# Optimization experiments

Measured on AMD Instinct MI355X. Metric: run time of the kernel, lower is better.

Reference implementation:

```python
import jax, jax.numpy as jnp
import numpy as np

B, T, D, H = 128, 64, 1024, 16
HD = D // H  # head dim = 64, matches smolgen per-pair bias last dim


def setup_inputs() -> dict:
    key = jax.random.key(0)
    ks = jax.random.split(key, 8)
    w = 0.02  # RandomNormal(stddev=0.02) init used throughout the repo
    return {
        "x": jax.random.normal(ks[0], (B, T, D), jnp.float32),
        # per-pair smolgen biases, shared across heads: [B, T, T, head_dim]
        "a_q": jax.random.normal(ks[1], (B, T, T, HD), jnp.float32) * 0.1,
        "a_k": jax.random.normal(ks[2], (B, T, T, HD), jnp.float32) * 0.1,
        "a_v": jax.random.normal(ks[3], (B, T, T, HD), jnp.float32) * 0.1,
        "Wq": jax.random.normal(ks[4], (D, D), jnp.float32) * w,
        "Wk": jax.random.normal(ks[5], (D, D), jnp.float32) * w,
        "Wv": jax.random.normal(ks[6], (D, D), jnp.float32) * w,
        "Wo": jax.random.normal(ks[7], (D, D), jnp.float32) * w,
    }


def reference(x, a_q, a_k, a_v, Wq, Wk, Wv, Wo):
    b, t, d_model = x.shape
    q = (x @ Wq).reshape(b, t, H, HD)
    k = (x @ Wk).reshape(b, t, H, HD)
    v = (x @ Wv).reshape(b, t, H, HD)
    scale = 1.0 / np.sqrt(HD).astype(np.float32)
    # standard content-content logits
    logits = jnp.einsum("bqhd,bkhd->bhqk", q, k) * scale
    # additive per-pair smolgen biases folded into QK^T (broadcast over heads)
    logits = logits + jnp.einsum("bqkd,bkhd->bhqk", a_q, k)
    logits = logits + jnp.einsum("bqhd,bqkd->bhqk", q, a_k)
    probs = jax.nn.softmax(logits, axis=-1)
    out = jnp.einsum("bhqk,bkhd->bqhd", probs, v)
    # per-pair value bias gathered by attention weights
    out = out + jnp.einsum("bhqk,bqkd->bqhd", probs, a_v)
    return out.reshape(b, t, d_model) @ Wo
```

## Files before the change

### kernel.cpp

```cpp
#include <hip/hip_runtime.h>
#include <hip/hip_bf16.h>

#define Bn 128
#define Tn 64
#define Dn 1024
#define Hn 16
#define HDn 64

typedef __bf16 bf16_t;
typedef __bf16 bf16x8 __attribute__((ext_vector_type(8)));
typedef float f32x4 __attribute__((ext_vector_type(4)));

__device__ __forceinline__ f32x4 mfma16(bf16x8 a, bf16x8 b, f32x4 c) {
  return __builtin_amdgcn_mfma_f32_16x16x32_bf16(a, b, c, 0, 0, 0);
}

__device__ __forceinline__ bf16x8 ld8f(const float* p) {
  float4 a = *(const float4*)p;
  float4 b = *(const float4*)(p + 4);
  bf16x8 r;
  r[0] = (bf16_t)a.x; r[1] = (bf16_t)a.y; r[2] = (bf16_t)a.z; r[3] = (bf16_t)a.w;
  r[4] = (bf16_t)b.x; r[5] = (bf16_t)b.y; r[6] = (bf16_t)b.z; r[7] = (bf16_t)b.w;
  return r;
}

__global__ __launch_bounds__(256) void convert_bf16(const float* __restrict__ src,
                                                    bf16_t* __restrict__ dst) {
  long i = ((long)blockIdx.x * 256 + threadIdx.x) * 8;
  *(bf16x8*)(dst + i) = ld8f(src + i);
}

__global__ __launch_bounds__(256) void transpose_mat(const float* __restrict__ W,
                                                     bf16_t* __restrict__ Wt) {
  __shared__ bf16_t tile[64][65];
  const int tr = blockIdx.y, tc = blockIdx.x;
  const int t = threadIdx.x;
#pragma unroll
  for (int i = 0; i < 16; i++) {
    int idx = t + i * 256;
    int r = idx >> 6, c = idx & 63;
    tile[r][c] = (bf16_t)W[(long)(tr * 64 + r) * 1024 + tc * 64 + c];
  }
  __syncthreads();
#pragma unroll
  for (int i = 0; i < 16; i++) {
    int idx = t + i * 256;
    int c = idx >> 6, r = idx & 63;
    Wt[(long)(tc * 64 + c) * 1024 + tr * 64 + r] = tile[r][c];
  }
}

template <typename CT>
__global__ __launch_bounds__(256) void gemm_bt(const bf16_t* __restrict__ A,
                                               const bf16_t* __restrict__ Bt,
                                               CT* __restrict__ C,
                                               int M, int N, int K) {
  __shared__ bf16_t As[128 * 64];
  __shared__ bf16_t Bs[128 * 64];
  const int t = threadIdx.x;
  const int w = t >> 6, lane = t & 63;
  const int l16 = lane & 15, quad = lane >> 4;
  const int m0 = blockIdx.y * 128, n0 = blockIdx.x * 128;
  const int wm = (w >> 1) * 64, wn = (w & 1) * 64;

  f32x4 acc[4][4];
#pragma unroll
  for (int i = 0; i < 4; i++)
#pragma unroll
    for (int j = 0; j < 4; j++) acc[i][j] = (f32x4){0.f, 0.f, 0.f, 0.f};

  const int sr = t >> 3;
  const int sc = (t & 7) * 8;

  for (int k0 = 0; k0 < K; k0 += 64) {
    __syncthreads();
#pragma unroll
    for (int i = 0; i < 4; i++) {
      int row = i * 32 + sr;
      *(bf16x8*)(As + row * 64 + sc) =
          *(const bf16x8*)(A + (long)(m0 + row) * K + k0 + sc);
      *(bf16x8*)(Bs + row * 64 + sc) =
          *(const bf16x8*)(Bt + (long)(n0 + row) * K + k0 + sc);
    }
    __syncthreads();
#pragma unroll
    for (int kk = 0; kk < 64; kk += 32) {
      bf16x8 af[4], bfr[4];
#pragma unroll
      for (int i = 0; i < 4; i++)
        af[i] = *(const bf16x8*)(As + (wm + i * 16 + l16) * 64 + kk + quad * 8);
#pragma unroll
      for (int j = 0; j < 4; j++)
        bfr[j] = *(const bf16x8*)(Bs + (wn + j * 16 + l16) * 64 + kk + quad * 8);
#pragma unroll
      for (int i = 0; i < 4; i++)
#pragma unroll
        for (int j = 0; j < 4; j++) acc[i][j] = mfma16(af[i], bfr[j], acc[i][j]);
    }
  }
#pragma unroll
  for (int i = 0; i < 4; i++)
#pragma unroll
    for (int j = 0; j < 4; j++) {
      int col = n0 + wn + j * 16 + l16;
#pragma unroll
      for (int r = 0; r < 4; r++) {
        int row = m0 + wm + i * 16 + quad * 4 + r;
        C[(long)row * N + col] = (CT)acc[i][j][r];
      }
    }
}

__global__ __launch_bounds__(256) void logits_cc(const bf16_t* __restrict__ Q,
                                                 const bf16_t* __restrict__ Km,
                                                 float* __restrict__ logits) {
  const int h = blockIdx.x, b = blockIdx.y;
  const int t = threadIdx.x, w = t >> 6, lane = t & 63;
  const int l16 = lane & 15, quad = lane >> 4;
  const bf16_t* qbase = Q + (long)b * (Tn * Dn) + h * HDn;
  const bf16_t* kbase = Km + (long)b * (Tn * Dn) + h * HDn;
  f32x4 acc[4];
#pragma unroll
  for (int j = 0; j < 4; j++) acc[j] = (f32x4){0.f, 0.f, 0.f, 0.f};
#pragma unroll
  for (int kk = 0; kk < 64; kk += 32) {
    bf16x8 af = *(const bf16x8*)(qbase + (long)(w * 16 + l16) * Dn + kk + quad * 8);
#pragma unroll
    for (int j = 0; j < 4; j++) {
      bf16x8 bfr = *(const bf16x8*)(kbase + (long)(j * 16 + l16) * Dn + kk + quad * 8);
      acc[j] = mfma16(af, bfr, acc[j]);
    }
  }
  float* lb = logits + ((long)(b * Hn + h) * Tn) * Tn;
#pragma unroll
  for (int j = 0; j < 4; j++)
#pragma unroll
    for (int r = 0; r < 4; r++) {
      int q = w * 16 + quad * 4 + r, k = j * 16 + l16;
      lb[q * 64 + k] = acc[j][r] * 0.125f;
    }
}

__global__ __launch_bounds__(256) void logits_aq(const float* __restrict__ aqp,
                                                 const bf16_t* __restrict__ Km,
                                                 float* __restrict__ logits) {
  const int b = blockIdx.y;
  const int kfix = blockIdx.x * 4 + (threadIdx.x >> 6);
  const int lane = threadIdx.x & 63, l16 = lane & 15, quad = lane >> 4;
  const float* abase = aqp + (long)b * (Tn * Tn * HDn) + kfix * HDn;
  const bf16_t* bbase = Km + (long)(b * Tn + kfix) * Dn;
  f32x4 acc[4];
#pragma unroll
  for (int i = 0; i < 4; i++) acc[i] = (f32x4){0.f, 0.f, 0.f, 0.f};
#pragma unroll
  for (int kk = 0; kk < 64; kk += 32) {
    bf16x8 bfr = *(const bf16x8*)(bbase + l16 * 64 + kk + quad * 8);
#pragma unroll
    for (int i = 0; i < 4; i++) {
      bf16x8 af = ld8f(abase + (long)(i * 16 + l16) * (Tn * HDn) + kk + quad * 8);
      acc[i] = mfma16(af, bfr, acc[i]);
    }
  }
  float* lb = logits + (long)b * (Hn * Tn * Tn) + kfix;
#pragma unroll
  for (int i = 0; i < 4; i++)
#pragma unroll
    for (int r = 0; r < 4; r++) {
      int q = i * 16 + quad * 4 + r, h = l16;
      lb[(long)h * (Tn * Tn) + q * Tn] += acc[i][r];
    }
}

__global__ __launch_bounds__(256) void logits_ak(const bf16_t* __restrict__ Q,
                                                 const float* __restrict__ akp,
                                                 float* __restrict__ logits) {
  const int b = blockIdx.y;
  const int q = blockIdx.x * 4 + (threadIdx.x >> 6);
  const int lane = threadIdx.x & 63, l16 = lane & 15, quad = lane >> 4;
  const bf16_t* abase = Q + (long)(b * Tn + q) * Dn;
  const float* bbase = akp + (long)(b * Tn + q) * (Tn * HDn);
  f32x4 acc[4];
#pragma unroll
  for (int j = 0; j < 4; j++) acc[j] = (f32x4){0.f, 0.f, 0.f, 0.f};
#pragma unroll
  for (int kk = 0; kk < 64; kk += 32) {
    bf16x8 af = *(const bf16x8*)(abase + l16 * 64 + kk + quad * 8);
#pragma unroll
    for (int j = 0; j < 4; j++) {
      bf16x8 bfr = ld8f(bbase + (long)(j * 16 + l16) * 64 + kk + quad * 8);
      acc[j] = mfma16(af, bfr, acc[j]);
    }
  }
  float* lb = logits + (long)b * (Hn * Tn * Tn) + q * 64;
#pragma unroll
  for (int j = 0; j < 4; j++)
#pragma unroll
    for (int r = 0; r < 4; r++) {
      int h = quad * 4 + r, k = j * 16 + l16;
      lb[(long)h * (Tn * Tn) + k] += acc[j][r];
    }
}

__global__ __launch_bounds__(256) void softmax_pav(const float* __restrict__ logits,
                                                   const float* __restrict__ avp,
                                                   bf16_t* __restrict__ probs,
                                                   bf16_t* __restrict__ out2) {
  const int q = blockIdx.x, b = blockIdx.y;
  __shared__ bf16_t pl[16][72];
  __shared__ bf16_t avT[64][72];
  const int t = threadIdx.x, w = t >> 6, lane = t & 63;
  const int l16 = lane & 15, quad = lane >> 4;

  {
    const float* src = avp + (long)(b * Tn + q) * (Tn * HDn);
    int k = t >> 2, d0 = (t & 3) * 16;
    unsigned short* lds = (unsigned short*)&avT[0][0];
#pragma unroll
    for (int c = 0; c < 4; c++) {
      float4 v = *(const float4*)(src + k * 64 + d0 + c * 4);
      bf16_t e0 = (bf16_t)v.x, e1 = (bf16_t)v.y, e2 = (bf16_t)v.z, e3 = (bf16_t)v.w;
      lds[(d0 + c * 4 + 0) * 72 + k] = *(unsigned short*)&e0;
      lds[(d0 + c * 4 + 1) * 72 + k] = *(unsigned short*)&e1;
      lds[(d0 + c * 4 + 2) * 72 + k] = *(unsigned short*)&e2;
      lds[(d0 + c * 4 + 3) * 72 + k] = *(unsigned short*)&e3;
    }
  }

  const int k = lane;
#pragma unroll
  for (int i = 0; i < 4; i++) {
    int h = w * 4 + i;
    float val = logits[((long)(b * Hn + h) * Tn + q) * Tn + k];
    float m = val;
#pragma unroll
    for (int off = 32; off; off >>= 1) m = fmaxf(m, __shfl_xor(m, off));
    float e = __expf(val - m);
    float s = e;
#pragma unroll
    for (int off = 32; off; off >>= 1) s += __shfl_xor(s, off);
    float p = e / s;
    bf16_t pb = (bf16_t)p;
    probs[((long)(b * Hn + h) * Tn + q) * Tn + k] = pb;
    pl[h][k] = pb;
  }
  __syncthreads();

  f32x4 acc = (f32x4){0.f, 0.f, 0.f, 0.f};
#pragma unroll
  for (int kk = 0; kk < 64; kk += 32) {
    bf16x8 af = *(const bf16x8*)(&pl[l16][kk + quad * 8]);
    bf16x8 bfr = *(const bf16x8*)(&avT[w * 16 + l16][kk + quad * 8]);
    acc = mfma16(af, bfr, acc);
  }
  bf16_t* ob = out2 + (long)(b * Tn + q) * Dn;
#pragma unroll
  for (int r = 0; r < 4; r++) {
    int h = quad * 4 + r, d = w * 16 + l16;
    ob[h * 64 + d] = (bf16_t)acc[r];
  }
}

__global__ __launch_bounds__(256) void pv_out(const bf16_t* __restrict__ probs,
                                              const bf16_t* __restrict__ V,
                                              const bf16_t* __restrict__ out2,
                                              bf16_t* __restrict__ attn) {
  const int h = blockIdx.x, b = blockIdx.y;
  __shared__ bf16_t VT[64][72];
  const int t = threadIdx.x, w = t >> 6, lane = t & 63;
  const int l16 = lane & 15, quad = lane >> 4;

  {
    const bf16_t* src = V + (long)b * (Tn * Dn) + h * HDn;
    int k = t & 63, d0 = (t >> 6) * 16;
    union { uint4 u; unsigned short s[8]; } v0, v1;
    v0.u = *(const uint4*)(src + (long)k * Dn + d0);
    v1.u = *(const uint4*)(src + (long)k * Dn + d0 + 8);
    unsigned short* lds = (unsigned short*)&VT[0][0];
#pragma unroll
    for (int j = 0; j < 8; j++) lds[(d0 + j) * 72 + k] = v0.s[j];
#pragma unroll
    for (int j = 0; j < 8; j++) lds[(d0 + 8 + j) * 72 + k] = v1.s[j];
  }
  __syncthreads();

  const bf16_t* pbase = probs + ((long)(b * Hn + h) * Tn) * Tn;
  f32x4 acc[4];
#pragma unroll
  for (int j = 0; j < 4; j++) acc[j] = (f32x4){0.f, 0.f, 0.f, 0.f};
#pragma unroll
  for (int kk = 0; kk < 64; kk += 32) {
    bf16x8 af = *(const bf16x8*)(pbase + (long)(w * 16 + l16) * Tn + kk + quad * 8);
#pragma unroll
    for (int j = 0; j < 4; j++) {
      bf16x8 bfr = *(const bf16x8*)(&VT[j * 16 + l16][kk + quad * 8]);
      acc[j] = mfma16(af, bfr, acc[j]);
    }
  }
#pragma unroll
  for (int j = 0; j < 4; j++)
#pragma unroll
    for (int r = 0; r < 4; r++) {
      int qrow = w * 16 + quad * 4 + r, d = j * 16 + l16;
      long idx = (long)(b * Tn + qrow) * Dn + h * HDn + d;
      attn[idx] = (bf16_t)(acc[j][r] + (float)out2[idx]);
    }
}

extern "C" void kernel_launch(void* const* d_in, const int* in_sizes, int n_in,
                              void* d_out, int out_size, void* d_ws, size_t ws_size,
                              hipStream_t stream) {
  const float* x  = (const float*)d_in[0];
  const float* aq = (const float*)d_in[1];
  const float* ak = (const float*)d_in[2];
  const float* av = (const float*)d_in[3];
  const float* Wq = (const float*)d_in[4];
  const float* Wk = (const float*)d_in[5];
  const float* Wv = (const float*)d_in[6];
  const float* Wo = (const float*)d_in[7];
  float* out = (float*)d_out;

  char* ws = (char*)d_ws;
  const size_t MB = 1024 * 1024;
  bf16_t* WqT    = (bf16_t*)(ws + 0 * MB);
  bf16_t* WkT    = (bf16_t*)(ws + 2 * MB);
  bf16_t* WvT    = (bf16_t*)(ws + 4 * MB);
  bf16_t* WoT    = (bf16_t*)(ws + 6 * MB);
  bf16_t* xb     = (bf16_t*)(ws + 8 * MB);
  bf16_t* Qb     = (bf16_t*)(ws + 24 * MB);
  bf16_t* Kb     = (bf16_t*)(ws + 40 * MB);
  bf16_t* Vb     = (bf16_t*)(ws + 56 * MB);
  float*  logits = (float*)(ws + 72 * MB);
  bf16_t* probs  = (bf16_t*)(ws + 104 * MB);
  bf16_t* out2   = (bf16_t*)(ws + 120 * MB);
  bf16_t* attn   = (bf16_t*)(ws + 136 * MB);

  dim3 blk(256);
  convert_bf16<<<dim3(4096), blk, 0, stream>>>(x, xb);
  transpose_mat<<<dim3(16, 16), blk, 0, stream>>>(Wq, WqT);
  transpose_mat<<<dim3(16, 16), blk, 0, stream>>>(Wk, WkT);
  transpose_mat<<<dim3(16, 16), blk, 0, stream>>>(Wv, WvT);
  transpose_mat<<<dim3(16, 16), blk, 0, stream>>>(Wo, WoT);

  gemm_bt<bf16_t><<<dim3(8, 64), blk, 0, stream>>>(xb, WqT, Qb, Bn * Tn, Dn, Dn);
  gemm_bt<bf16_t><<<dim3(8, 64), blk, 0, stream>>>(xb, WkT, Kb, Bn * Tn, Dn, Dn);
  gemm_bt<bf16_t><<<dim3(8, 64), blk, 0, stream>>>(xb, WvT, Vb, Bn * Tn, Dn, Dn);

  logits_cc<<<dim3(Hn, Bn), blk, 0, stream>>>(Qb, Kb, logits);
  logits_aq<<<dim3(16, Bn), blk, 0, stream>>>(aq, Kb, logits);
  logits_ak<<<dim3(16, Bn), blk, 0, stream>>>(Qb, ak, logits);

  softmax_pav<<<dim3(Tn, Bn), blk, 0, stream>>>(logits, av, probs, out2);
  pv_out<<<dim3(Hn, Bn), blk, 0, stream>>>(probs, Vb, out2, attn);

  gemm_bt<float><<<dim3(8, 64), blk, 0, stream>>>(attn, WoT, out, Bn * Tn, Dn, Dn);
}
```

Measured before the change: 649.2 us.

## Fuse logit bias terms, softmax and value-bias gather into one attention kernel

Replaces the three logit kernels and the softmax/value-bias kernel with a single 1024-thread kernel per (batch, 16-query tile). The fp32 logits now stay in shared memory instead of round-tripping through a 32 MB global buffer with read-modify-write passes. The kernel also uses swizzled LDS layouts for the probabilities and the transposed value bias. In exchange it uses large shared memory (about 100 KB) and 1024-thread blocks, which limits occupancy, and it adds several block-wide barriers.

```diff
diff --git a/kernel.cpp b/kernel.cpp
--- a/kernel.cpp
+++ b/kernel.cpp
@@ -111,152 +111,159 @@
     }
 }
 
-__global__ __launch_bounds__(256) void logits_cc(const bf16_t* __restrict__ Q,
-                                                 const bf16_t* __restrict__ Km,
-                                                 float* __restrict__ logits) {
-  const int h = blockIdx.x, b = blockIdx.y;
-  const int t = threadIdx.x, w = t >> 6, lane = t & 63;
-  const int l16 = lane & 15, quad = lane >> 4;
-  const bf16_t* qbase = Q + (long)b * (Tn * Dn) + h * HDn;
-  const bf16_t* kbase = Km + (long)b * (Tn * Dn) + h * HDn;
-  f32x4 acc[4];
-#pragma unroll
-  for (int j = 0; j < 4; j++) acc[j] = (f32x4){0.f, 0.f, 0.f, 0.f};
-#pragma unroll
-  for (int kk = 0; kk < 64; kk += 32) {
-    bf16x8 af = *(const bf16x8*)(qbase + (long)(w * 16 + l16) * Dn + kk + quad * 8);
-#pragma unroll
-    for (int j = 0; j < 4; j++) {
-      bf16x8 bfr = *(const bf16x8*)(kbase + (long)(j * 16 + l16) * Dn + kk + quad * 8);
-      acc[j] = mfma16(af, bfr, acc[j]);
-    }
-  }
-  float* lb = logits + ((long)(b * Hn + h) * Tn) * Tn;
-#pragma unroll
-  for (int j = 0; j < 4; j++)
-#pragma unroll
-    for (int r = 0; r < 4; r++) {
-      int q = w * 16 + quad * 4 + r, k = j * 16 + l16;
-      lb[q * 64 + k] = acc[j][r] * 0.125f;
-    }
-}
-
-__global__ __launch_bounds__(256) void logits_aq(const float* __restrict__ aqp,
-                                                 const bf16_t* __restrict__ Km,
-                                                 float* __restrict__ logits) {
-  const int b = blockIdx.y;
-  const int kfix = blockIdx.x * 4 + (threadIdx.x >> 6);
-  const int lane = threadIdx.x & 63, l16 = lane & 15, quad = lane >> 4;
-  const float* abase = aqp + (long)b * (Tn * Tn * HDn) + kfix * HDn;
-  const bf16_t* bbase = Km + (long)(b * Tn + kfix) * Dn;
-  f32x4 acc[4];
-#pragma unroll
-  for (int i = 0; i < 4; i++) acc[i] = (f32x4){0.f, 0.f, 0.f, 0.f};
-#pragma unroll
-  for (int kk = 0; kk < 64; kk += 32) {
-    bf16x8 bfr = *(const bf16x8*)(bbase + l16 * 64 + kk + quad * 8);
-#pragma unroll
-    for (int i = 0; i < 4; i++) {
-      bf16x8 af = ld8f(abase + (long)(i * 16 + l16) * (Tn * HDn) + kk + quad * 8);
-      acc[i] = mfma16(af, bfr, acc[i]);
-    }
-  }
-  float* lb = logits + (long)b * (Hn * Tn * Tn) + kfix;
-#pragma unroll
-  for (int i = 0; i < 4; i++)
-#pragma unroll
-    for (int r = 0; r < 4; r++) {
-      int q = i * 16 + quad * 4 + r, h = l16;
-      lb[(long)h * (Tn * Tn) + q * Tn] += acc[i][r];
-    }
-}
-
-__global__ __launch_bounds__(256) void logits_ak(const bf16_t* __restrict__ Q,
-                                                 const float* __restrict__ akp,
-                                                 float* __restrict__ logits) {
-  const int b = blockIdx.y;
-  const int q = blockIdx.x * 4 + (threadIdx.x >> 6);
-  const int lane = threadIdx.x & 63, l16 = lane & 15, quad = lane >> 4;
-  const bf16_t* abase = Q + (long)(b * Tn + q) * Dn;
-  const float* bbase = akp + (long)(b * Tn + q) * (Tn * HDn);
-  f32x4 acc[4];
-#pragma unroll
-  for (int j = 0; j < 4; j++) acc[j] = (f32x4){0.f, 0.f, 0.f, 0.f};
-#pragma unroll
-  for (int kk = 0; kk < 64; kk += 32) {
-    bf16x8 af = *(const bf16x8*)(abase + l16 * 64 + kk + quad * 8);
-#pragma unroll
-    for (int j = 0; j < 4; j++) {
-      bf16x8 bfr = ld8f(bbase + (long)(j * 16 + l16) * 64 + kk + quad * 8);
-      acc[j] = mfma16(af, bfr, acc[j]);
-    }
-  }
-  float* lb = logits + (long)b * (Hn * Tn * Tn) + q * 64;
-#pragma unroll
-  for (int j = 0; j < 4; j++)
-#pragma unroll
-    for (int r = 0; r < 4; r++) {
-      int h = quad * 4 + r, k = j * 16 + l16;
-      lb[(long)h * (Tn * Tn) + k] += acc[j][r];
-    }
-}
-
-__global__ __launch_bounds__(256) void softmax_pav(const float* __restrict__ logits,
-                                                   const float* __restrict__ avp,
-                                                   bf16_t* __restrict__ probs,
-                                                   bf16_t* __restrict__ out2) {
-  const int q = blockIdx.x, b = blockIdx.y;
-  __shared__ bf16_t pl[16][72];
-  __shared__ bf16_t avT[64][72];
-  const int t = threadIdx.x, w = t >> 6, lane = t & 63;
-  const int l16 = lane & 15, quad = lane >> 4;
-
-  {
-    const float* src = avp + (long)(b * Tn + q) * (Tn * HDn);
-    int k = t >> 2, d0 = (t & 3) * 16;
-    unsigned short* lds = (unsigned short*)&avT[0][0];
-#pragma unroll
-    for (int c = 0; c < 4; c++) {
-      float4 v = *(const float4*)(src + k * 64 + d0 + c * 4);
-      bf16_t e0 = (bf16_t)v.x, e1 = (bf16_t)v.y, e2 = (bf16_t)v.z, e3 = (bf16_t)v.w;
-      lds[(d0 + c * 4 + 0) * 72 + k] = *(unsigned short*)&e0;
-      lds[(d0 + c * 4 + 1) * 72 + k] = *(unsigned short*)&e1;
-      lds[(d0 + c * 4 + 2) * 72 + k] = *(unsigned short*)&e2;
-      lds[(d0 + c * 4 + 3) * 72 + k] = *(unsigned short*)&e3;
-    }
-  }
-
-  const int k = lane;
-#pragma unroll
-  for (int i = 0; i < 4; i++) {
-    int h = w * 4 + i;
-    float val = logits[((long)(b * Hn + h) * Tn + q) * Tn + k];
-    float m = val;
-#pragma unroll
-    for (int off = 32; off; off >>= 1) m = fmaxf(m, __shfl_xor(m, off));
-    float e = __expf(val - m);
-    float s = e;
-#pragma unroll
-    for (int off = 32; off; off >>= 1) s += __shfl_xor(s, off);
-    float p = e / s;
-    bf16_t pb = (bf16_t)p;
-    probs[((long)(b * Hn + h) * Tn + q) * Tn + k] = pb;
-    pl[h][k] = pb;
-  }
-  __syncthreads();
-
-  f32x4 acc = (f32x4){0.f, 0.f, 0.f, 0.f};
-#pragma unroll
-  for (int kk = 0; kk < 64; kk += 32) {
-    bf16x8 af = *(const bf16x8*)(&pl[l16][kk + quad * 8]);
-    bf16x8 bfr = *(const bf16x8*)(&avT[w * 16 + l16][kk + quad * 8]);
-    acc = mfma16(af, bfr, acc);
-  }
-  bf16_t* ob = out2 + (long)(b * Tn + q) * Dn;
-#pragma unroll
-  for (int r = 0; r < 4; r++) {
-    int h = quad * 4 + r, d = w * 16 + l16;
-    ob[h * 64 + d] = (bf16_t)acc[r];
+__global__ __launch_bounds__(1024) void fused_att(
+    const bf16_t* __restrict__ Qb, const bf16_t* __restrict__ Kb,
+    const float* __restrict__ aqp, const float* __restrict__ akp,
+    const float* __restrict__ avp,
+    bf16_t* __restrict__ probs, bf16_t* __restrict__ out2) {
+  __shared__ float Ls[256 * 65];
+  __shared__ bf16_t Pb[256 * 64];
+
+  const int id = blockIdx.x;
+  const int b = (id & 7) * 16 + ((id >> 3) & 15);
+  const int q0 = (id >> 7) * 16;
+  const int t = threadIdx.x;
+  const int w = t >> 6, lane = t & 63, l16 = lane & 15, quad = lane >> 4;
+
+  {
+    const int h = w;
+    f32x4 acc[4];
+#pragma unroll
+    for (int j = 0; j < 4; j++) acc[j] = (f32x4){0.f, 0.f, 0.f, 0.f};
+    const bf16_t* qb = Qb + (long)(b * Tn + q0 + l16) * Dn + h * HDn;
+    const bf16_t* kb = Kb + (long)b * (Tn * Dn) + h * HDn;
+#pragma unroll
+    for (int kk = 0; kk < 64; kk += 32) {
+      bf16x8 af = *(const bf16x8*)(qb + kk + quad * 8);
+#pragma unroll
+      for (int j = 0; j < 4; j++) {
+        bf16x8 bf = *(const bf16x8*)(kb + (long)(j * 16 + l16) * Dn + kk + quad * 8);
+        acc[j] = mfma16(af, bf, acc[j]);
+      }
+    }
+#pragma unroll
+    for (int j = 0; j < 4; j++)
+#pragma unroll
+      for (int r = 0; r < 4; r++)
+        Ls[((quad * 4 + r) * 16 + h) * 65 + j * 16 + l16] = 0.125f * acc[j][r];
+  }
+  __syncthreads();
+
+  {
+    const float* ab = aqp + (long)(b * Tn + q0 + l16) * (Tn * HDn);
+    const bf16_t* kb = Kb + (long)b * (Tn * Dn) + l16 * HDn;
+#pragma unroll
+    for (int kc = 0; kc < 4; kc++) {
+      const int k = w * 4 + kc;
+      f32x4 acc = (f32x4){0.f, 0.f, 0.f, 0.f};
+#pragma unroll
+      for (int kk = 0; kk < 64; kk += 32) {
+        bf16x8 af = ld8f(ab + k * HDn + kk + quad * 8);
+        bf16x8 bf = *(const bf16x8*)(kb + (long)k * Dn + kk + quad * 8);
+        acc = mfma16(af, bf, acc);
+      }
+#pragma unroll
+      for (int r = 0; r < 4; r++)
+        Ls[((quad * 4 + r) * 16 + l16) * 65 + k] += acc[r];
+    }
+  }
+  __syncthreads();
+
+  {
+    const int q = w;
+    const bf16_t* qb = Qb + (long)(b * Tn + q0 + q) * Dn + l16 * HDn;
+    const float* ab = akp + (long)(b * Tn + q0 + q) * (Tn * HDn);
+    f32x4 acc[4];
+#pragma unroll
+    for (int j = 0; j < 4; j++) acc[j] = (f32x4){0.f, 0.f, 0.f, 0.f};
+#pragma unroll
+    for (int kk = 0; kk < 64; kk += 32) {
+      bf16x8 af = *(const bf16x8*)(qb + kk + quad * 8);
+#pragma unroll
+      for (int j = 0; j < 4; j++) {
+        bf16x8 bf = ld8f(ab + (long)(j * 16 + l16) * HDn + kk + quad * 8);
+        acc[j] = mfma16(af, bf, acc[j]);
+      }
+    }
+#pragma unroll
+    for (int j = 0; j < 4; j++)
+#pragma unroll
+      for (int r = 0; r < 4; r++)
+        Ls[(q * 16 + quad * 4 + r) * 65 + j * 16 + l16] += acc[j][r];
+  }
+  __syncthreads();
+
+  {
+    const int r = t >> 2, qq = t & 3;
+    const int q = r >> 4, h = r & 15;
+    const float* row = Ls + r * 65 + qq * 16;
+    float m = -1e30f;
+#pragma unroll
+    for (int i = 0; i < 16; i++) m = fmaxf(m, row[i]);
+    m = fmaxf(m, __shfl_xor(m, 1));
+    m = fmaxf(m, __shfl_xor(m, 2));
+    float e[16];
+    float s = 0.f;
+#pragma unroll
+    for (int i = 0; i < 16; i++) { e[i] = __expf(row[i] - m); s += e[i]; }
+    s += __shfl_xor(s, 1);
+    s += __shfl_xor(s, 2);
+    const float inv = 1.0f / s;
+    const int swz = (q ^ h) & 7;
+    bf16_t* pr = probs + ((long)(b * Hn + h) * Tn + q0 + q) * Tn + qq * 16;
+#pragma unroll
+    for (int c = 0; c < 2; c++) {
+      bf16x8 v;
+#pragma unroll
+      for (int ee = 0; ee < 8; ee++) v[ee] = (bf16_t)(e[c * 8 + ee] * inv);
+      *(bf16x8*)(pr + c * 8) = v;
+      const int cg = qq * 2 + c;
+      *(bf16x8*)(Pb + r * 64 + (cg ^ swz) * 8) = v;
+    }
+  }
+
+  {
+    const int q = w;
+    bf16_t* avT = (bf16_t*)(Ls + 16 * w * 65);
+    const float* src = avp + (long)(b * Tn + q0 + q) * (Tn * HDn) + lane * HDn;
+    f32x4 acc[4];
+#pragma unroll
+    for (int j = 0; j < 4; j++) acc[j] = (f32x4){0.f, 0.f, 0.f, 0.f};
+    const int aswz = (q ^ l16) & 7;
+#pragma unroll
+    for (int half = 0; half < 2; half++) {
+      asm volatile("s_waitcnt lgkmcnt(0)" ::: "memory");
+#pragma unroll
+      for (int c = 0; c < 8; c++) {
+        float4 v = *(const float4*)(src + half * 32 + c * 4);
+#pragma unroll
+        for (int ee = 0; ee < 4; ee++) {
+          int dl = c * 4 + ee;
+          avT[dl * 64 + (((lane >> 3) ^ dl) & 7) * 8 + (lane & 7)] =
+              (bf16_t)(&v.x)[ee];
+        }
+      }
+      asm volatile("s_waitcnt lgkmcnt(0)" ::: "memory");
+      __builtin_amdgcn_sched_barrier(0);
+#pragma unroll
+      for (int kk = 0; kk < 64; kk += 32) {
+        const int cg = (kk >> 3) + quad;
+        bf16x8 af = *(const bf16x8*)(Pb + (q * 16 + l16) * 64 + (cg ^ aswz) * 8);
+#pragma unroll
+        for (int jj = 0; jj < 2; jj++) {
+          int j = half * 2 + jj;
+          int dl = jj * 16 + l16;
+          bf16x8 bf = *(const bf16x8*)(avT + dl * 64 + ((cg ^ (dl & 7))) * 8);
+          acc[j] = mfma16(af, bf, acc[j]);
+        }
+      }
+    }
+    bf16_t* ob = out2 + (long)(b * Tn + q0 + q) * Dn;
+#pragma unroll
+    for (int j = 0; j < 4; j++)
+#pragma unroll
+      for (int r = 0; r < 4; r++)
+        ob[(quad * 4 + r) * HDn + j * 16 + l16] = (bf16_t)acc[j][r];
   }
 }
 
@@ -329,10 +336,9 @@
   bf16_t* Qb     = (bf16_t*)(ws + 24 * MB);
   bf16_t* Kb     = (bf16_t*)(ws + 40 * MB);
   bf16_t* Vb     = (bf16_t*)(ws + 56 * MB);
-  float*  logits = (float*)(ws + 72 * MB);
-  bf16_t* probs  = (bf16_t*)(ws + 104 * MB);
-  bf16_t* out2   = (bf16_t*)(ws + 120 * MB);
-  bf16_t* attn   = (bf16_t*)(ws + 136 * MB);
+  bf16_t* probs  = (bf16_t*)(ws + 72 * MB);
+  bf16_t* out2   = (bf16_t*)(ws + 88 * MB);
+  bf16_t* attn   = (bf16_t*)(ws + 104 * MB);
 
   dim3 blk(256);
   convert_bf16<<<dim3(4096), blk, 0, stream>>>(x, xb);
@@ -345,11 +351,8 @@
   gemm_bt<bf16_t><<<dim3(8, 64), blk, 0, stream>>>(xb, WkT, Kb, Bn * Tn, Dn, Dn);
   gemm_bt<bf16_t><<<dim3(8, 64), blk, 0, stream>>>(xb, WvT, Vb, Bn * Tn, Dn, Dn);
 
-  logits_cc<<<dim3(Hn, Bn), blk, 0, stream>>>(Qb, Kb, logits);
-  logits_aq<<<dim3(16, Bn), blk, 0, stream>>>(aq, Kb, logits);
-  logits_ak<<<dim3(16, Bn), blk, 0, stream>>>(Qb, ak, logits);
-
-  softmax_pav<<<dim3(Tn, Bn), blk, 0, stream>>>(logits, av, probs, out2);
+  fused_att<<<dim3(512), dim3(1024), 0, stream>>>(Qb, Kb, aq, ak, av, probs, out2);
+
   pv_out<<<dim3(Hn, Bn), blk, 0, stream>>>(probs, Vb, out2, attn);
 
   gemm_bt<float><<<dim3(8, 64), blk, 0, stream>>>(attn, WoT, out, Bn * Tn, Dn, Dn);
```

Result: faster. 577.9 us (-11.0%).
